# Kernel tuning notes

Measured on AMD Instinct MI355X. Metric: run time of the kernel, lower is better.

Reference implementation:

```python
import jax, jax.numpy as jnp
import numpy as np

B, C, W = 8, 128, 4096
REDUCTION = 8
D = C // REDUCTION  # 16


def setup_inputs() -> dict:
    key = jax.random.key(0)
    ks = jax.random.split(key, 7)
    scale = 0.05
    return {
        "x": jax.random.normal(ks[0], (B, C, W), dtype=jnp.float32),
        "Wq": jax.random.normal(ks[1], (D, C), dtype=jnp.float32) * scale,
        "bq": jax.random.normal(ks[2], (D,), dtype=jnp.float32) * scale,
        "Wk": jax.random.normal(ks[3], (D, C), dtype=jnp.float32) * scale,
        "bk": jax.random.normal(ks[4], (D,), dtype=jnp.float32) * scale,
        "Wv": jax.random.normal(ks[5], (C, C), dtype=jnp.float32) * scale,
        "bv": jax.random.normal(ks[6], (C,), dtype=jnp.float32) * scale,
    }


def reference(x, Wq, bq, Wk, bk, Wv, bv):
    # 1x1 Conv1d == per-position linear over channel axis
    q = jnp.einsum('dc,bcw->bdw', Wq, x) + bq[None, :, None]   # [B, D, W]
    k = jnp.einsum('dc,bcw->bdw', Wk, x) + bk[None, :, None]   # [B, D, W]
    v = jnp.einsum('oc,bcw->bow', Wv, x) + bv[None, :, None]   # [B, C, W]
    scale = D ** (-0.5)
    # scores[b,i,j] = q[b,:,i] . k[b,:,j]
    scores = jnp.einsum('bdi,bdj->bij', q, k) * scale          # [B, W, W]
    attn = jax.nn.softmax(scores, axis=-1)
    # torch.bmm(value, attn): context[b,c,w] = sum_j v[b,c,j] * attn[b,j,w]
    context = jnp.einsum('bcj,bjw->bcw', v, attn)              # [B, C, W]
    return context + x
```

## Files before the change

kernel.cpp:

```cpp
#include <hip/hip_runtime.h>

#define B_ 8
#define C_ 128
#define W_ 4096
#define D_ 16
#define SCALE2 0.3606737602222409f

typedef short bf16x8 __attribute__((ext_vector_type(8)));
typedef float f32x4 __attribute__((ext_vector_type(4)));

__device__ __forceinline__ unsigned short f2bf(float f) {
    unsigned int u = __float_as_uint(f);
    u += 0x7fffu + ((u >> 16) & 1u);
    return (unsigned short)(u >> 16);
}
__device__ __forceinline__ unsigned int pk2bf(float lo, float hi) {
    return __builtin_amdgcn_perm(__float_as_uint(hi), __float_as_uint(lo), 0x07060302u);
}
__device__ __forceinline__ bf16x8 u4_to_bf8(unsigned int a, unsigned int b,
                                            unsigned int c, unsigned int d) {
    union { uint4 u; bf16x8 v; } t;
    t.u = make_uint4(a, b, c, d);
    return t.v;
}
__device__ __forceinline__ int xswz(int j, int c8) {
    return c8 ^ (j & 7) ^ ((j >> 3) & 7);
}

__global__ __launch_bounds__(256) void prep(
    const float* __restrict__ Wq, const float* __restrict__ Wk, const float* __restrict__ Wv,
    unsigned short* __restrict__ Wvbf, unsigned short* __restrict__ Wqkbf)
{
    int g = blockIdx.x * 256 + threadIdx.x;
    const float* src; unsigned short* dst; float sc = 1.0f;
    if (g < 4096)      { src = Wv + g * 4;            dst = Wvbf + g * 4; }
    else if (g < 4608) { int t = g - 4096; src = Wq + t * 4; dst = Wqkbf + t * 4; sc = SCALE2; }
    else               { int t = g - 4608; src = Wk + t * 4; dst = Wqkbf + 2048 + t * 4; }
    float4 v = *(const float4*)src;
    unsigned short h[4] = {f2bf(v.x * sc), f2bf(v.y * sc), f2bf(v.z * sc), f2bf(v.w * sc)};
    *(ushort4*)dst = *(ushort4*)h;
}

__global__ __launch_bounds__(256) void proj(
    const float* __restrict__ x, const unsigned short* __restrict__ Wvbf,
    const unsigned short* __restrict__ Wqkbf,
    const float* __restrict__ bqp, const float* __restrict__ bkp, const float* __restrict__ bvp,
    unsigned short* __restrict__ qws, unsigned short* __restrict__ kws,
    unsigned short* __restrict__ vws)
{
    __shared__ unsigned short xbf[64 * 128];
    __shared__ unsigned short outs[128 * 72];

    int b  = blockIdx.x & 7;
    int j0 = (blockIdx.x >> 3) * 64;
    int tid = threadIdx.x;
    int wid = tid >> 6, lane = tid & 63, n = lane & 15, q4 = lane >> 4;

#pragma unroll
    for (int i = 0; i < 8; i++) {
        int c = (tid >> 4) + 16 * i;
        int jc = (tid & 15) * 4;
        float4 t = *(const float4*)(x + (size_t)(b * C_ + c) * W_ + j0 + jc);
        float tv[4] = {t.x, t.y, t.z, t.w};
#pragma unroll
        for (int cc = 0; cc < 4; cc++) {
            int j = jc + cc;
            xbf[j * 128 + xswz(j, c >> 3) * 8 + (c & 7)] = f2bf(tv[cc]);
        }
    }
    __syncthreads();

    const f32x4 zero = {0.f, 0.f, 0.f, 0.f};
    f32x4 accv[2][4]; f32x4 accq = zero, acck = zero;
#pragma unroll
    for (int os = 0; os < 2; os++)
#pragma unroll
        for (int js = 0; js < 4; js++) accv[os][js] = zero;

#pragma unroll
    for (int kk = 0; kk < 128; kk += 32) {
        bf16x8 av[2], aqf, akf, bx[4];
#pragma unroll
        for (int os = 0; os < 2; os++)
            av[os] = *(const bf16x8*)(Wvbf + (wid * 32 + os * 16 + n) * 128 + kk + q4 * 8);
        aqf = *(const bf16x8*)(Wqkbf + n * 128 + kk + q4 * 8);
        akf = *(const bf16x8*)(Wqkbf + (16 + n) * 128 + kk + q4 * 8);
#pragma unroll
        for (int js = 0; js < 4; js++) {
            int j = js * 16 + n;
            bx[js] = *(const bf16x8*)&xbf[j * 128 + xswz(j, (kk >> 3) + q4) * 8];
        }
#pragma unroll
        for (int os = 0; os < 2; os++)
#pragma unroll
            for (int js = 0; js < 4; js++)
                accv[os][js] = __builtin_amdgcn_mfma_f32_16x16x32_bf16(av[os], bx[js], accv[os][js], 0, 0, 0);
        accq = __builtin_amdgcn_mfma_f32_16x16x32_bf16(aqf, bx[wid], accq, 0, 0, 0);
        acck = __builtin_amdgcn_mfma_f32_16x16x32_bf16(akf, bx[wid], acck, 0, 0, 0);
    }

    {
        int pos = j0 + wid * 16 + n;
        float q0 = accq[0] + bqp[q4 * 4 + 0] * SCALE2;
        float q1 = accq[1] + bqp[q4 * 4 + 1] * SCALE2;
        float q2 = accq[2] + bqp[q4 * 4 + 2] * SCALE2;
        float q3 = accq[3] + bqp[q4 * 4 + 3] * SCALE2;
        float k0 = acck[0] + bkp[q4 * 4 + 0];
        float k1 = acck[1] + bkp[q4 * 4 + 1];
        float k2 = acck[2] + bkp[q4 * 4 + 2];
        float k3 = acck[3] + bkp[q4 * 4 + 3];
        size_t base = ((size_t)(b * 4 + (q4 >> 1)) * W_ + pos) * 8 + (q4 & 1) * 4;
        *(uint2*)(qws + base) = make_uint2((unsigned)f2bf(q0) | ((unsigned)f2bf(q1) << 16),
                                           (unsigned)f2bf(q2) | ((unsigned)f2bf(q3) << 16));
        *(uint2*)(kws + base) = make_uint2((unsigned)f2bf(k0) | ((unsigned)f2bf(k1) << 16),
                                           (unsigned)f2bf(k2) | ((unsigned)f2bf(k3) << 16));
    }
    {
        int which = tid >> 7;
        int plane = 2 + ((tid >> 6) & 1);
        int pos = j0 + (tid & 63);
        unsigned short* basep = which ? kws : qws;
        uint4 z = make_uint4(0, 0, 0, 0);
        if (which == 1 && plane == 2) z.x = 0x3f80u;
        *(uint4*)(basep + ((size_t)(b * 4 + plane) * W_ + pos) * 8) = z;
    }

    float bvv[2][4];
#pragma unroll
    for (int os = 0; os < 2; os++)
#pragma unroll
        for (int r = 0; r < 4; r++) bvv[os][r] = bvp[wid * 32 + os * 16 + q4 * 4 + r];
#pragma unroll
    for (int os = 0; os < 2; os++)
#pragma unroll
        for (int js = 0; js < 4; js++)
#pragma unroll
            for (int r = 0; r < 4; r++) {
                int c = wid * 32 + os * 16 + q4 * 4 + r;
                int j = js * 16 + n;
                outs[c * 72 + j] = f2bf(accv[os][js][r] + bvv[os][r]);
            }
    __syncthreads();
    {
        int p = tid;
#pragma unroll
        for (int rep = 0; rep < 2; rep++, p += 256) {
            int jt_l = p >> 7;
            int c    = p & 127;
            const uint4* src = (const uint4*)&outs[c * 72 + jt_l * 16];
            unsigned short* dst = vws + ((size_t)((b * 256 + (j0 >> 4) + jt_l) * 128 + c)) * 16;
            *(uint4*)(dst + 0) = src[0];
            *(uint4*)(dst + 8) = src[1];
        }
    }
}

__global__ __launch_bounds__(256) void row_stats(
    unsigned short* __restrict__ qws, const unsigned short* __restrict__ kws)
{
    int b  = blockIdx.x & 7;
    int j0 = (blockIdx.x >> 3) * 64;
    int tid = threadIdx.x;
    int wid = tid >> 6, lane = tid & 63, n = lane & 15, q4 = lane >> 4;

    const bf16x8* qbase = (const bf16x8*)qws + (size_t)(b * 4 + q4) * W_;
    const bf16x8* kbase = (const bf16x8*)kws + (size_t)(b * 4 + q4) * W_;
    bf16x8 aq = qbase[j0 + wid * 16 + n];
    const f32x4 zero = {0.f, 0.f, 0.f, 0.f};

    float lt[4] = {0.f, 0.f, 0.f, 0.f};
    bf16x8 bkc[4];
#pragma unroll
    for (int ws = 0; ws < 4; ws++) bkc[ws] = kbase[ws * 16 + n];

    for (int t = 0; t < W_ / 64; t++) {
        f32x4 s[4];
#pragma unroll
        for (int ws = 0; ws < 4; ws++)
            s[ws] = __builtin_amdgcn_mfma_f32_16x16x32_bf16(aq, bkc[ws], zero, 0, 0, 0);
        int tn = (t + 1) & 63;
#pragma unroll
        for (int ws = 0; ws < 4; ws++) bkc[ws] = kbase[tn * 64 + ws * 16 + n];
#pragma unroll
        for (int ws = 0; ws < 4; ws++)
#pragma unroll
            for (int r = 0; r < 4; r++) lt[r] += __builtin_amdgcn_exp2f(s[ws][r]);
    }
#pragma unroll
    for (int mask = 1; mask < 16; mask <<= 1)
#pragma unroll
        for (int r = 0; r < 4; r++) lt[r] += __shfl_xor(lt[r], mask, 64);
    if (n == 0) {
#pragma unroll
        for (int r = 0; r < 4; r++) {
            int j = j0 + wid * 16 + q4 * 4 + r;
            qws[((size_t)(b * 4 + 2) * W_ + j) * 8] = f2bf(-__builtin_amdgcn_logf(lt[r]));
        }
    }
}

__global__ __launch_bounds__(256, 2) void attn_out(
    const float* __restrict__ x, const unsigned short* __restrict__ qws,
    const unsigned short* __restrict__ kws, const unsigned short* __restrict__ vws,
    float* __restrict__ out)
{
    __shared__ float red[2][128 * 68];

    int b  = blockIdx.x & 7;
    int w0 = (blockIdx.x >> 3) * 64;
    int tid = threadIdx.x;
    int wid = tid >> 6, lane = tid & 63, n = lane & 15, q4 = lane >> 4;

    const bf16x8* qbase = (const bf16x8*)qws + (size_t)(b * 4 + q4) * W_;
    const bf16x8* kbase = (const bf16x8*)kws + (size_t)(b * 4 + q4) * W_;
    const unsigned short* vtb = vws + (size_t)b * 256 * 128 * 16;

    bf16x8 bk[4];
#pragma unroll
    for (int ws = 0; ws < 4; ws++) bk[ws] = kbase[w0 + ws * 16 + n];

    const f32x4 zero = {0.f, 0.f, 0.f, 0.f};
    f32x4 acc[8][4];
#pragma unroll
    for (int mt = 0; mt < 8; mt++)
#pragma unroll
        for (int nt = 0; nt < 4; nt++) acc[mt][nt] = zero;

    bf16x8 aqA = qbase[wid * 16 + n];
    bf16x8 aqB = qbase[64 + wid * 16 + n];

    for (int it = 0; it < 32; it++) {
        f32x4 sA[4], sB[4];
#pragma unroll
        for (int ws = 0; ws < 4; ws++) {
            sA[ws] = __builtin_amdgcn_mfma_f32_16x16x32_bf16(aqA, bk[ws], zero, 0, 0, 0);
            sB[ws] = __builtin_amdgcn_mfma_f32_16x16x32_bf16(aqB, bk[ws], zero, 0, 0, 0);
        }
        int itn = (it + 1) & 31;
        bf16x8 aqA_n = qbase[itn * 128 + wid * 16 + n];
        bf16x8 aqB_n = qbase[itn * 128 + 64 + wid * 16 + n];

        bf16x8 bfrag[4];
#pragma unroll
        for (int ws = 0; ws < 4; ws++) {
            float pA0 = __builtin_amdgcn_exp2f(sA[ws][0]);
            float pA1 = __builtin_amdgcn_exp2f(sA[ws][1]);
            float pA2 = __builtin_amdgcn_exp2f(sA[ws][2]);
            float pA3 = __builtin_amdgcn_exp2f(sA[ws][3]);
            float pB0 = __builtin_amdgcn_exp2f(sB[ws][0]);
            float pB1 = __builtin_amdgcn_exp2f(sB[ws][1]);
            float pB2 = __builtin_amdgcn_exp2f(sB[ws][2]);
            float pB3 = __builtin_amdgcn_exp2f(sB[ws][3]);
            bfrag[ws] = u4_to_bf8(pk2bf(pA0, pA1), pk2bf(pA2, pA3),
                                  pk2bf(pB0, pB1), pk2bf(pB2, pB3));
        }

        int jtA = it * 8 + wid;
        int jtB = jtA + 4;
#pragma unroll
        for (int mt = 0; mt < 8; mt++) {
            int c = mt * 16 + n;
            uint2 a0 = *(const uint2*)(vtb + (size_t)(jtA * 128 + c) * 16 + q4 * 4);
            uint2 a1 = *(const uint2*)(vtb + (size_t)(jtB * 128 + c) * 16 + q4 * 4);
            bf16x8 af = u4_to_bf8(a0.x, a0.y, a1.x, a1.y);
#pragma unroll
            for (int nt = 0; nt < 4; nt++)
                acc[mt][nt] = __builtin_amdgcn_mfma_f32_16x16x32_bf16(af, bfrag[nt], acc[mt][nt], 0, 0, 0);
        }
        aqA = aqA_n; aqB = aqB_n;
    }

#pragma unroll 1
    for (int step = 0; step < 1; step++) {}

    if (wid >= 2) {
        float* buf = red[wid - 2];
#pragma unroll
        for (int mt = 0; mt < 8; mt++)
#pragma unroll
            for (int nt = 0; nt < 4; nt++)
#pragma unroll
                for (int r = 0; r < 4; r++)
                    buf[(mt * 16 + q4 * 4 + r) * 68 + nt * 16 + n] = acc[mt][nt][r];
    }
    __syncthreads();
    if (wid < 2) {
        const float* buf = red[wid];
#pragma unroll
        for (int mt = 0; mt < 8; mt++)
#pragma unroll
            for (int nt = 0; nt < 4; nt++)
#pragma unroll
                for (int r = 0; r < 4; r++)
                    acc[mt][nt][r] += buf[(mt * 16 + q4 * 4 + r) * 68 + nt * 16 + n];
    }
    __syncthreads();
    if (wid == 1) {
        float* buf = red[0];
#pragma unroll
        for (int mt = 0; mt < 8; mt++)
#pragma unroll
            for (int nt = 0; nt < 4; nt++)
#pragma unroll
                for (int r = 0; r < 4; r++)
                    buf[(mt * 16 + q4 * 4 + r) * 68 + nt * 16 + n] = acc[mt][nt][r];
    }
    __syncthreads();
    if (wid == 0) {
        float* buf = red[0];
#pragma unroll
        for (int mt = 0; mt < 8; mt++)
#pragma unroll
            for (int nt = 0; nt < 4; nt++)
#pragma unroll
                for (int r = 0; r < 4; r++) {
                    int idx = (mt * 16 + q4 * 4 + r) * 68 + nt * 16 + n;
                    buf[idx] = acc[mt][nt][r] + buf[idx];
                }
    }
    __syncthreads();
    {
#pragma unroll
        for (int u = 0; u < 8; u++) {
            int k = tid + 256 * u;
            int c = k >> 4, wseg = (k & 15) * 4;
            size_t gidx = (size_t)(b * C_ + c) * W_ + w0 + wseg;
            float4 xv = *(const float4*)(x + gidx);
            const float* s = &red[0][c * 68 + wseg];
            float4 o = make_float4(s[0] + xv.x, s[1] + xv.y, s[2] + xv.z, s[3] + xv.w);
            *(float4*)(out + gidx) = o;
        }
    }
}

extern "C" void kernel_launch(void* const* d_in, const int* in_sizes, int n_in,
                              void* d_out, int out_size, void* d_ws, size_t ws_size,
                              hipStream_t stream)
{
    const float* x  = (const float*)d_in[0];
    const float* Wq = (const float*)d_in[1];
    const float* bq = (const float*)d_in[2];
    const float* Wk = (const float*)d_in[3];
    const float* bk = (const float*)d_in[4];
    const float* Wv = (const float*)d_in[5];
    const float* bv = (const float*)d_in[6];
    float* out = (float*)d_out;

    unsigned short* qws  = (unsigned short*)d_ws;
    unsigned short* kws  = qws + (size_t)1048576;
    unsigned short* vws  = kws + (size_t)1048576;
    unsigned short* Wvbf = vws + (size_t)4194304;
    unsigned short* Wqkbf = Wvbf + 16384;

    prep<<<20, 256, 0, stream>>>(Wq, Wk, Wv, Wvbf, Wqkbf);
    proj<<<512, 256, 0, stream>>>(x, Wvbf, Wqkbf, bq, bk, bv, qws, kws, vws);
    row_stats<<<512, 256, 0, stream>>>(qws, kws);
    attn_out<<<512, 256, 0, stream>>>(x, qws, kws, vws, out);
}
```

Measured before the change: 167.9 us.

## Split row_stats over key chunks and software-pipeline attn_out V loads and exp

row_stats is split across four key-range chunks, giving four times as many blocks. Each chunk writes partial exp sums to a float workspace, and a new finl kernel sums them and writes the log-normalizer into qws. attn_out is restructured into a software pipeline: the V fragments for the next iteration are prefetched into registers, and the exp/pack of the scores is computed one iteration ahead so it can overlap the PV MFMAs. This adds an extra launch and more register pressure in attn_out, which uses launch_bounds of 2 blocks per CU, so occupancy or spilling could suffer.

Measured after the change: 167.3 us. About the same (-0.3%).

```diff
diff --git a/kernel.cpp b/kernel.cpp
--- a/kernel.cpp
+++ b/kernel.cpp
@@ -22,6 +22,13 @@
     union { uint4 u; bf16x8 v; } t;
     t.u = make_uint4(a, b, c, d);
     return t.v;
+}
+__device__ __forceinline__ bf16x8 exp2pack(f32x4 a, f32x4 b) {
+    return u4_to_bf8(
+        pk2bf(__builtin_amdgcn_exp2f(a[0]), __builtin_amdgcn_exp2f(a[1])),
+        pk2bf(__builtin_amdgcn_exp2f(a[2]), __builtin_amdgcn_exp2f(a[3])),
+        pk2bf(__builtin_amdgcn_exp2f(b[0]), __builtin_amdgcn_exp2f(b[1])),
+        pk2bf(__builtin_amdgcn_exp2f(b[2]), __builtin_amdgcn_exp2f(b[3])));
 }
 __device__ __forceinline__ int xswz(int j, int c8) {
     return c8 ^ (j & 7) ^ ((j >> 3) & 7);
@@ -156,10 +163,14 @@
 }
 
 __global__ __launch_bounds__(256) void row_stats(
-    unsigned short* __restrict__ qws, const unsigned short* __restrict__ kws)
-{
-    int b  = blockIdx.x & 7;
-    int j0 = (blockIdx.x >> 3) * 64;
+    const unsigned short* __restrict__ qws, const unsigned short* __restrict__ kws,
+    float* __restrict__ rlp)
+{
+    int blk = blockIdx.x;
+    int b = blk & 7;
+    int j0 = ((blk >> 3) & 63) * 64;
+    int wsp = blk >> 9;
+    int t0 = wsp * 16;
     int tid = threadIdx.x;
     int wid = tid >> 6, lane = tid & 63, n = lane & 15, q4 = lane >> 4;
 
@@ -169,34 +180,53 @@
     const f32x4 zero = {0.f, 0.f, 0.f, 0.f};
 
     float lt[4] = {0.f, 0.f, 0.f, 0.f};
-    bf16x8 bkc[4];
-#pragma unroll
-    for (int ws = 0; ws < 4; ws++) bkc[ws] = kbase[ws * 16 + n];
-
-    for (int t = 0; t < W_ / 64; t++) {
-        f32x4 s[4];
+    bf16x8 k0[4], k1[4];
+#pragma unroll
+    for (int ws = 0; ws < 4; ws++) {
+        k0[ws] = kbase[(t0 + 0) * 64 + ws * 16 + n];
+        k1[ws] = kbase[(t0 + 1) * 64 + ws * 16 + n];
+    }
+
+#pragma unroll 2
+    for (int t = 0; t < 8; t++) {
+        f32x4 sa[4], sb[4];
 #pragma unroll
         for (int ws = 0; ws < 4; ws++)
-            s[ws] = __builtin_amdgcn_mfma_f32_16x16x32_bf16(aq, bkc[ws], zero, 0, 0, 0);
-        int tn = (t + 1) & 63;
-#pragma unroll
-        for (int ws = 0; ws < 4; ws++) bkc[ws] = kbase[tn * 64 + ws * 16 + n];
+            sa[ws] = __builtin_amdgcn_mfma_f32_16x16x32_bf16(aq, k0[ws], zero, 0, 0, 0);
 #pragma unroll
         for (int ws = 0; ws < 4; ws++)
-#pragma unroll
-            for (int r = 0; r < 4; r++) lt[r] += __builtin_amdgcn_exp2f(s[ws][r]);
+            sb[ws] = __builtin_amdgcn_mfma_f32_16x16x32_bf16(aq, k1[ws], zero, 0, 0, 0);
+        int ta = t0 + ((2 * t + 2) & 15), tb = t0 + ((2 * t + 3) & 15);
+#pragma unroll
+        for (int ws = 0; ws < 4; ws++) {
+            k0[ws] = kbase[ta * 64 + ws * 16 + n];
+            k1[ws] = kbase[tb * 64 + ws * 16 + n];
+        }
+#pragma unroll
+        for (int ws = 0; ws < 4; ws++)
+#pragma unroll
+            for (int r = 0; r < 4; r++) {
+                lt[r] += __builtin_amdgcn_exp2f(sa[ws][r]);
+                lt[r] += __builtin_amdgcn_exp2f(sb[ws][r]);
+            }
     }
 #pragma unroll
     for (int mask = 1; mask < 16; mask <<= 1)
 #pragma unroll
         for (int r = 0; r < 4; r++) lt[r] += __shfl_xor(lt[r], mask, 64);
     if (n == 0) {
-#pragma unroll
-        for (int r = 0; r < 4; r++) {
-            int j = j0 + wid * 16 + q4 * 4 + r;
-            qws[((size_t)(b * 4 + 2) * W_ + j) * 8] = f2bf(-__builtin_amdgcn_logf(lt[r]));
-        }
-    }
+        f32x4 l4 = {lt[0], lt[1], lt[2], lt[3]};
+        *(f32x4*)(rlp + (size_t)wsp * 32768 + (size_t)b * W_ + j0 + wid * 16 + q4 * 4) = l4;
+    }
+}
+
+__global__ __launch_bounds__(256) void finl(const float* __restrict__ rlp,
+                                            unsigned short* __restrict__ qws)
+{
+    int g = blockIdx.x * 256 + threadIdx.x;
+    int b = g >> 12, j = g & (W_ - 1);
+    float l = rlp[g] + rlp[32768 + g] + rlp[65536 + g] + rlp[98304 + g];
+    qws[((size_t)(b * 4 + 2) * W_ + j) * 8] = f2bf(-__builtin_amdgcn_logf(l));
 }
 
 __global__ __launch_bounds__(256, 2) void attn_out(
@@ -228,50 +258,55 @@
 
     bf16x8 aqA = qbase[wid * 16 + n];
     bf16x8 aqB = qbase[64 + wid * 16 + n];
+    uint2 vfA[8], vfB[8];
+#pragma unroll
+    for (int mt = 0; mt < 8; mt++) {
+        int c = mt * 16 + n;
+        vfA[mt] = *(const uint2*)(vtb + (size_t)((wid) * 128 + c) * 16 + q4 * 4);
+        vfB[mt] = *(const uint2*)(vtb + (size_t)((wid + 4) * 128 + c) * 16 + q4 * 4);
+    }
+    f32x4 sA[4], sB[4];
+#pragma unroll
+    for (int ws = 0; ws < 4; ws++) {
+        sA[ws] = __builtin_amdgcn_mfma_f32_16x16x32_bf16(aqA, bk[ws], zero, 0, 0, 0);
+        sB[ws] = __builtin_amdgcn_mfma_f32_16x16x32_bf16(aqB, bk[ws], zero, 0, 0, 0);
+    }
+    aqA = qbase[128 + wid * 16 + n];
+    aqB = qbase[128 + 64 + wid * 16 + n];
+    bf16x8 bfrag[4];
+#pragma unroll
+    for (int ws = 0; ws < 4; ws++) bfrag[ws] = exp2pack(sA[ws], sB[ws]);
 
     for (int it = 0; it < 32; it++) {
-        f32x4 sA[4], sB[4];
+        int itn = (it + 1) & 31;
+        uint2 vfA_n[8], vfB_n[8];
+        int jtA_n = itn * 8 + wid, jtB_n = jtA_n + 4;
+#pragma unroll
+        for (int mt = 0; mt < 8; mt++) {
+            int c = mt * 16 + n;
+            vfA_n[mt] = *(const uint2*)(vtb + (size_t)(jtA_n * 128 + c) * 16 + q4 * 4);
+            vfB_n[mt] = *(const uint2*)(vtb + (size_t)(jtB_n * 128 + c) * 16 + q4 * 4);
+        }
 #pragma unroll
         for (int ws = 0; ws < 4; ws++) {
             sA[ws] = __builtin_amdgcn_mfma_f32_16x16x32_bf16(aqA, bk[ws], zero, 0, 0, 0);
             sB[ws] = __builtin_amdgcn_mfma_f32_16x16x32_bf16(aqB, bk[ws], zero, 0, 0, 0);
         }
-        int itn = (it + 1) & 31;
-        bf16x8 aqA_n = qbase[itn * 128 + wid * 16 + n];
-        bf16x8 aqB_n = qbase[itn * 128 + 64 + wid * 16 + n];
-
-        bf16x8 bfrag[4];
-#pragma unroll
-        for (int ws = 0; ws < 4; ws++) {
-            float pA0 = __builtin_amdgcn_exp2f(sA[ws][0]);
-            float pA1 = __builtin_amdgcn_exp2f(sA[ws][1]);
-            float pA2 = __builtin_amdgcn_exp2f(sA[ws][2]);
-            float pA3 = __builtin_amdgcn_exp2f(sA[ws][3]);
-            float pB0 = __builtin_amdgcn_exp2f(sB[ws][0]);
-            float pB1 = __builtin_amdgcn_exp2f(sB[ws][1]);
-            float pB2 = __builtin_amdgcn_exp2f(sB[ws][2]);
-            float pB3 = __builtin_amdgcn_exp2f(sB[ws][3]);
-            bfrag[ws] = u4_to_bf8(pk2bf(pA0, pA1), pk2bf(pA2, pA3),
-                                  pk2bf(pB0, pB1), pk2bf(pB2, pB3));
-        }
-
-        int jtA = it * 8 + wid;
-        int jtB = jtA + 4;
+        int itn2 = (it + 2) & 31;
+        aqA = qbase[itn2 * 128 + wid * 16 + n];
+        aqB = qbase[itn2 * 128 + 64 + wid * 16 + n];
 #pragma unroll
         for (int mt = 0; mt < 8; mt++) {
-            int c = mt * 16 + n;
-            uint2 a0 = *(const uint2*)(vtb + (size_t)(jtA * 128 + c) * 16 + q4 * 4);
-            uint2 a1 = *(const uint2*)(vtb + (size_t)(jtB * 128 + c) * 16 + q4 * 4);
-            bf16x8 af = u4_to_bf8(a0.x, a0.y, a1.x, a1.y);
+            bf16x8 af = u4_to_bf8(vfA[mt].x, vfA[mt].y, vfB[mt].x, vfB[mt].y);
 #pragma unroll
             for (int nt = 0; nt < 4; nt++)
                 acc[mt][nt] = __builtin_amdgcn_mfma_f32_16x16x32_bf16(af, bfrag[nt], acc[mt][nt], 0, 0, 0);
         }
-        aqA = aqA_n; aqB = aqB_n;
-    }
-
-#pragma unroll 1
-    for (int step = 0; step < 1; step++) {}
+#pragma unroll
+        for (int ws = 0; ws < 4; ws++) bfrag[ws] = exp2pack(sA[ws], sB[ws]);
+#pragma unroll
+        for (int mt = 0; mt < 8; mt++) { vfA[mt] = vfA_n[mt]; vfB[mt] = vfB_n[mt]; }
+    }
 
     if (wid >= 2) {
         float* buf = red[wid - 2];
@@ -351,9 +386,11 @@
     unsigned short* vws  = kws + (size_t)1048576;
     unsigned short* Wvbf = vws + (size_t)4194304;
     unsigned short* Wqkbf = Wvbf + 16384;
+    float* rlp = (float*)(Wqkbf + 4096);
 
     prep<<<20, 256, 0, stream>>>(Wq, Wk, Wv, Wvbf, Wqkbf);
     proj<<<512, 256, 0, stream>>>(x, Wvbf, Wqkbf, bq, bk, bv, qws, kws, vws);
-    row_stats<<<512, 256, 0, stream>>>(qws, kws);
+    row_stats<<<2048, 256, 0, stream>>>(qws, kws, rlp);
+    finl<<<128, 256, 0, stream>>>(rlp, qws);
     attn_out<<<512, 256, 0, stream>>>(x, qws, kws, vws, out);
 }
```
